# Kernel tuning notes

Hardware: AMD Instinct MI355X
Metric: run time of the kernel (lower is better)

## Reference

```python
import jax, jax.numpy as jnp
import numpy as np

B, C, O, N, T, K = 4, 64, 64, 32768, 4, 9
PAD, DIL = 4, 1  # padding*dilation, dilation
SIGMA = 0.05
EPS_BN = 1e-5


def _gather_ch(x, idx):
    # x: [B, C, N], idx: [B, N] -> gather along last dim per channel
    idx3 = jnp.broadcast_to(idx[:, None, :], x.shape)
    return jnp.take_along_axis(x, idx3, axis=-1)


def _weighted_conv(x, coords, w):
    # x: [B,C,N], coords: [B,3,N], w: [O,C,K]
    xp = jnp.pad(x, ((0, 0), (0, 0), (PAD, PAD)))
    cp = jnp.pad(coords, ((0, 0), (0, 0), (PAD, PAD)))
    win_idx = jnp.arange(N)[:, None] + jnp.arange(K) * DIL  # [N, K]
    win = xp[:, :, win_idx]   # [B,C,N,K]
    cwin = cp[:, :, win_idx]  # [B,3,N,K]
    d = cwin - cwin[:, :, :, K // 2:K // 2 + 1]
    s = jnp.sum(d * d, axis=1)                    # [B,N,K]
    r = jnp.sqrt(jnp.where(s > 0, s, 1.0))
    r = jnp.where(s > 0, r, 0.0)
    wgt = jnp.maximum(1.0 - r / SIGMA, 0.0)       # [B,N,K]
    return jnp.einsum('bcnk,bnk,ock->bon', win, wgt, w)


def _bn(x, g, b):
    # training-mode BatchNorm1d over (B, N)
    m = jnp.mean(x, axis=(0, 2), keepdims=True)
    v = jnp.var(x, axis=(0, 2), keepdims=True)
    return g[None, :, None] * (x - m) * jax.lax.rsqrt(v + EPS_BN) + b[None, :, None]


def setup_inputs() -> dict:
    key = jax.random.key(0)
    ks = jax.random.split(key, 12)
    inp = jax.random.normal(ks[0], (B, C, N), dtype=jnp.float32)
    # coords in a small box so sigma=0.05 yields non-trivial weights
    multi_coords = jax.random.uniform(ks[1], (B, 3, N, T), dtype=jnp.float32) * 0.02
    indices = jax.random.randint(ks[2], (B, N, T), 0, N, dtype=jnp.int32)
    reindices = jax.random.randint(ks[3], (B, N, T), 0, N, dtype=jnp.int32)
    fan = C * K
    conv_w = jax.random.normal(ks[4], (T, O, C, K), dtype=jnp.float32) / np.sqrt(fan)
    bn_gamma = jnp.ones((T, O), dtype=jnp.float32)
    bn_beta = jnp.zeros((T, O), dtype=jnp.float32)
    fusion_w = jax.random.normal(ks[5], (O, T * O), dtype=jnp.float32) / np.sqrt(T * O)
    fusion_b = jnp.zeros((O,), dtype=jnp.float32)
    fusion_gamma = jnp.ones((O,), dtype=jnp.float32)
    fusion_beta = jnp.zeros((O,), dtype=jnp.float32)
    return {"input": inp, "multi_coords": multi_coords, "indices": indices,
            "reindices": reindices, "conv_w": conv_w, "bn_gamma": bn_gamma,
            "bn_beta": bn_beta, "fusion_w": fusion_w, "fusion_b": fusion_b,
            "fusion_gamma": fusion_gamma, "fusion_beta": fusion_beta}


def reference(input, multi_coords, indices, reindices, conv_w, bn_gamma, bn_beta,
              fusion_w, fusion_b, fusion_gamma, fusion_beta):
    outs = []
    for i in range(T):  # fixed small set of 4 Hilbert orders
        x = _gather_ch(input, indices[:, :, i])            # [B,C,N]
        x = _weighted_conv(x, multi_coords[:, :, :, i], conv_w[i])  # [B,O,N]
        x = _bn(x, bn_gamma[i], bn_beta[i])
        x = _gather_ch(x, reindices[:, :, i])
        outs.append(x)
    cat = jnp.concatenate(outs, axis=1)                    # [B, T*O, N]
    y = jnp.einsum('bcn,oc->bon', cat, fusion_w) + fusion_b[None, :, None]
    y = _bn(y, fusion_gamma, fusion_beta)
    return jax.nn.relu(y)
```

## Files before the change

### kernel.cpp

```cpp
#include <hip/hip_runtime.h>
#include <hip/hip_bf16.h>

#define BB 4
#define CC 64
#define OO 64
#define NN 32768
#define TT 4
#define KK 9
#define PADW 4
#define SIGMA 0.05f
#define EPS_BN 1e-5f

typedef __attribute__((ext_vector_type(8))) short bf16x8;
typedef __attribute__((ext_vector_type(4))) float f32x4;

__device__ __forceinline__ unsigned short f2bf(float f) {
  __hip_bfloat16 h = __float2bfloat16(f);
  return *reinterpret_cast<unsigned short*>(&h);
}
__device__ __forceinline__ unsigned int pkbf(float a, float b) {
  float2 t; t.x = a; t.y = b;
  __hip_bfloat162 h = __float22bfloat162_rn(t);
  unsigned int r;
  __builtin_memcpy(&r, &h, 4);
  return r;
}

__global__ __launch_bounds__(256) void transpose_kernel(
    const float* __restrict__ inp, unsigned short* __restrict__ xTb)
{
  const int n0 = blockIdx.x * 64;
  const int b  = blockIdx.y;
  const int tid = threadIdx.x;
  __shared__ float xt[64][65];
  {
    int nl = tid & 63, c4 = tid >> 6;
    #pragma unroll
    for (int i = 0; i < 16; ++i) {
      int c = c4 * 16 + i;
      xt[c][nl] = inp[((size_t)(b*CC + c))*NN + n0 + nl];
    }
  }
  __syncthreads();
  {
    int nl = tid >> 2, cq = tid & 3;
    unsigned int pk[8];
    #pragma unroll
    for (int i = 0; i < 8; ++i) {
      int c = cq*16 + i*2;
      pk[i] = pkbf(xt[c][nl], xt[c+1][nl]);
    }
    unsigned int* dst = (unsigned int*)(xTb + (((size_t)b*NN) + n0 + nl)*CC + cq*16);
    ((int4*)dst)[0] = make_int4((int)pk[0],(int)pk[1],(int)pk[2],(int)pk[3]);
    ((int4*)dst)[1] = make_int4((int)pk[4],(int)pk[5],(int)pk[6],(int)pk[7]);
  }
}

__global__ __launch_bounds__(256) void wprep_kernel(
    const float* __restrict__ cw, unsigned short* __restrict__ W4)
{
  const int k = blockIdx.x;
  const int t = blockIdx.y;
  for (int u = threadIdx.x; u < OO*CC; u += 256) {
    int o = u >> 6, c = u & 63;
    int ow = o >> 5, ot = (o >> 4) & 1, l15 = o & 15;
    int frag = c >> 5, q = (c >> 3) & 3, j = c & 7;
    float wv = cw[(((size_t)(t*OO + o))*CC + c)*KK + k];
    W4[(size_t)(t*9+k)*4096 + ow*2048 + ot*1024 + frag*512 + l15*32 + q*8 + j]
        = f2bf(wv);
  }
}

__global__ __launch_bounds__(256) void indmc_kernel(
    const int* __restrict__ ind, const float* __restrict__ mc,
    int* __restrict__ indT, float* __restrict__ mcT)
{
  const int n = blockIdx.x * 256 + threadIdx.x;
  const int b = blockIdx.y;
  int4 iv = *(const int4*)(ind + ((size_t)b*NN + n)*TT);
  indT[((size_t)(0*BB + b))*NN + n] = iv.x;
  indT[((size_t)(1*BB + b))*NN + n] = iv.y;
  indT[((size_t)(2*BB + b))*NN + n] = iv.z;
  indT[((size_t)(3*BB + b))*NN + n] = iv.w;
  #pragma unroll
  for (int d = 0; d < 3; ++d) {
    float4 mv = *(const float4*)(mc + (((size_t)(b*3 + d))*NN + n)*TT);
    mcT[((size_t)((0*BB + b)*3 + d))*NN + n] = mv.x;
    mcT[((size_t)((1*BB + b)*3 + d))*NN + n] = mv.y;
    mcT[((size_t)((2*BB + b)*3 + d))*NN + n] = mv.z;
    mcT[((size_t)((3*BB + b)*3 + d))*NN + n] = mv.w;
  }
}

__global__ __launch_bounds__(256, 3) void conv_kernel(
    const unsigned short* __restrict__ xTb,
    const float* __restrict__ mcT,
    const int*   __restrict__ indT,
    const unsigned short* __restrict__ W4,
    unsigned short* __restrict__ Y,
    float* __restrict__ cpart2)
{
  const int n0  = blockIdx.x * 256;
  const int b   = blockIdx.y;
  const int t   = blockIdx.z;
  const int tid = threadIdx.x;
  const int lane = tid & 63;
  const int w    = tid >> 6;
  const int l15  = lane & 15;
  const int q    = lane >> 4;
  const int ow   = w & 1;
  const int nw   = w >> 1;

  __shared__ short xg[264*64];
  __shared__ float wgl[256][10];
  __shared__ float mcs[3][268];
  __shared__ int   ids[268];

  for (int u = tid; u < 264; u += 256) {
    int m = n0 + u - PADW;
    bool v = (m >= 0) && (m < NN);
    ids[u] = v ? indT[((size_t)(t*BB + b))*NN + m] : -1;
    #pragma unroll
    for (int d = 0; d < 3; ++d)
      mcs[d][u] = v ? mcT[((size_t)((t*BB + b)*3 + d))*NN + m] : 0.f;
  }
  __syncthreads();

  int4 g[9];
  #pragma unroll
  for (int i = 0; i < 9; ++i) {
    int u = tid + 256*i;
    g[i] = make_int4(0,0,0,0);
    if (u < 2112) {
      int p = u >> 3, s = u & 7;
      int idx = ids[p];
      if (idx >= 0)
        g[i] = *(const int4*)(xTb + ((size_t)b*NN + idx)*CC + s*8);
    }
  }

  {
    int nl = tid;
    float cx = mcs[0][nl+4], cy = mcs[1][nl+4], cz = mcs[2][nl+4];
    #pragma unroll
    for (int k = 0; k < KK; ++k) {
      float dx = mcs[0][nl+k]-cx, dy = mcs[1][nl+k]-cy, dz = mcs[2][nl+k]-cz;
      float s2 = dx*dx + dy*dy + dz*dz;
      float r = (s2 > 0.f) ? sqrtf(s2) : 0.f;
      wgl[nl][k] = fmaxf(1.f - r*(1.f/SIGMA), 0.f);
    }
  }

  #pragma unroll
  for (int i = 0; i < 9; ++i) {
    int u = tid + 256*i;
    if (u < 2112) {
      int p = u >> 3, s = u & 7;
      *(int4*)&xg[(p << 6) + ((s ^ (p & 7)) << 3)] = g[i];
    }
  }
  __syncthreads();

  const unsigned short* Wt = W4 + (size_t)t*9*4096 + ow*2048 + (l15*4 + q)*8;
  const f32x4 Z = {0.f, 0.f, 0.f, 0.f};
  f32x4 fin[2][8];
  #pragma unroll
  for (int ot = 0; ot < 2; ++ot)
    #pragma unroll
    for (int ns = 0; ns < 8; ++ns) fin[ot][ns] = Z;

  for (int k = 0; k < KK; ++k) {
    const unsigned short* Wk = Wt + (size_t)k*4096;
    bf16x8 af[2][2];
    #pragma unroll
    for (int ot = 0; ot < 2; ++ot) {
      af[ot][0] = *(const bf16x8*)(Wk + ot*1024);
      af[ot][1] = *(const bf16x8*)(Wk + ot*1024 + 512);
    }
    #pragma unroll
    for (int ns = 0; ns < 8; ++ns) {
      int nl = nw*128 + ns*16 + l15;
      int p  = nl + k;
      const short* row = &xg[p << 6];
      int sw = p & 7;
      bf16x8 b0 = *(const bf16x8*)(row + ((q ^ sw) << 3));
      bf16x8 b1 = *(const bf16x8*)(row + (((4 + q) ^ sw) << 3));
      float wgt = wgl[nl][k];
      #pragma unroll
      for (int ot = 0; ot < 2; ++ot) {
        f32x4 d = __builtin_amdgcn_mfma_f32_16x16x32_bf16(af[ot][0], b0, Z, 0, 0, 0);
        d = __builtin_amdgcn_mfma_f32_16x16x32_bf16(af[ot][1], b1, d, 0, 0, 0);
        fin[ot][ns] += wgt * d;
      }
    }
  }

  #pragma unroll
  for (int ns = 0; ns < 8; ++ns) {
    int nl = nw*128 + ns*16 + l15;
    size_t row = (((size_t)t*BB + b)*NN + n0 + nl)*OO;
    #pragma unroll
    for (int ot = 0; ot < 2; ++ot) {
      uint2 pk2;
      pk2.x = pkbf(fin[ot][ns][0], fin[ot][ns][1]);
      pk2.y = pkbf(fin[ot][ns][2], fin[ot][ns][3]);
      *(uint2*)(Y + row + ow*32 + ot*16 + q*4) = pk2;
    }
  }

  float sv[16];
  #pragma unroll
  for (int ot = 0; ot < 2; ++ot)
    #pragma unroll
    for (int r = 0; r < 4; ++r) {
      float a = 0.f, qs = 0.f;
      #pragma unroll
      for (int ns = 0; ns < 8; ++ns) {
        float v = fin[ot][ns][r];
        a += v; qs += v*v;
      }
      sv[ot*4+r] = a; sv[8+ot*4+r] = qs;
    }
  #pragma unroll
  for (int msk = 1; msk < 16; msk <<= 1) {
    #pragma unroll
    for (int i = 0; i < 16; ++i) sv[i] += __shfl_xor(sv[i], msk, 16);
  }
  if (l15 == 0) {
    int slot4 = ((b*128 + (int)blockIdx.x) << 2) | w;
    #pragma unroll
    for (int ot = 0; ot < 2; ++ot)
      #pragma unroll
      for (int r = 0; r < 4; ++r) {
        int o = ow*32 + ot*16 + q*4 + r;
        cpart2[((size_t)((t*64 + o)*2 + 0))*2048 + slot4] = sv[ot*4+r];
        cpart2[((size_t)((t*64 + o)*2 + 1))*2048 + slot4] = sv[8+ot*4+r];
      }
  }
}

__global__ __launch_bounds__(256) void bnparam_kernel(
    const float* __restrict__ cpart2,
    const float* __restrict__ gam,
    const float* __restrict__ bet,
    float* __restrict__ ss)
{
  const int to = blockIdx.x;
  const int tid = threadIdx.x;
  __shared__ float r1[256], r2[256];
  const float* p1 = cpart2 + (size_t)to*2*2048;
  const float* p2 = p1 + 2048;
  float s1 = 0.f, s2 = 0.f;
  for (int i = tid*4; i < 2048; i += 1024) {
    float4 a = *(const float4*)(p1 + i);
    float4 c = *(const float4*)(p2 + i);
    s1 += a.x + a.y + a.z + a.w;
    s2 += c.x + c.y + c.z + c.w;
  }
  r1[tid] = s1; r2[tid] = s2;
  __syncthreads();
  for (int st = 128; st > 0; st >>= 1) {
    if (tid < st) { r1[tid] += r1[tid+st]; r2[tid] += r2[tid+st]; }
    __syncthreads();
  }
  if (tid == 0) {
    const float inv = 1.f / (float)(BB * NN);
    float mean = r1[0] * inv;
    float var  = r2[0] * inv - mean * mean;
    float sc = gam[to] * rsqrtf(var + EPS_BN);
    ss[to*2 + 0] = sc;
    ss[to*2 + 1] = bet[to] - mean * sc;
  }
}

__global__ __launch_bounds__(256) void wfuse_kernel(
    const float* __restrict__ fw,
    const float* __restrict__ fb,
    const float* __restrict__ ss,
    float* __restrict__ fbp,
    unsigned short* __restrict__ FWB)
{
  const int tid = threadIdx.x;
  {
    int o = tid >> 2, c0 = (tid & 3) * 64;
    float s = 0.f;
    for (int c = c0; c < c0 + 64; ++c)
      s += fw[o*256 + c] * ss[c*2 + 1];
    s += __shfl_xor(s, 1);
    s += __shfl_xor(s, 2);
    if ((tid & 3) == 0) fbp[o] = fb[o] + s;
  }
  for (int e = tid; e < 16384; e += 256) {
    int rk  = e >> 11;
    int ow  = (e >> 10) & 1;
    int ot  = (e >> 9) & 1;
    int l15 = (e >> 5) & 15;
    int cj  = e & 31;
    int o = ow*32 + ot*16 + l15;
    int c = (rk >> 1)*64 + (rk & 1)*32 + cj;
    FWB[e] = f2bf(fw[o*256 + c] * ss[c*2]);
  }
}

__global__ __launch_bounds__(256, 6) void fusion_kernel(
    const unsigned short* __restrict__ Y,
    const int*   __restrict__ rind,
    const unsigned short* __restrict__ FWB,
    const float* __restrict__ fbp,
    float* __restrict__ out,
    float* __restrict__ fpart2)
{
  const int n0  = blockIdx.x * 128;
  const int b   = blockIdx.y;
  const int tid = threadIdx.x;
  const int lane = tid & 63;
  const int w    = tid >> 6;
  const int l15  = lane & 15;
  const int q    = lane >> 4;
  const int ow   = w & 1;
  const int nw   = w >> 1;

  __shared__ short zg[128*64];

  int4 rg[4];
  #pragma unroll
  for (int i = 0; i < 4; ++i) {
    int n = (tid >> 3) + 32*i;
    rg[i] = *(const int4*)(rind + ((size_t)b*NN + n0 + n)*TT);
  }

  f32x4 fin[2][4];
  #pragma unroll
  for (int ot = 0; ot < 2; ++ot)
    #pragma unroll
    for (int ns = 0; ns < 4; ++ns) fin[ot][ns] = (f32x4){0.f,0.f,0.f,0.f};

  #pragma unroll
  for (int r = 0; r < 4; ++r) {
    if (r) __syncthreads();
    #pragma unroll
    for (int i = 0; i < 4; ++i) {
      int u = tid + 256*i;
      int n = u >> 3, s = u & 7;
      int rn = (r == 0) ? rg[i].x : (r == 1) ? rg[i].y
             : (r == 2) ? rg[i].z : rg[i].w;
      int4 raw = *(const int4*)(Y + (((size_t)r*BB + b)*NN + rn)*OO + s*8);
      *(int4*)&zg[(n << 6) + ((s ^ (n & 7)) << 3)] = raw;
    }
    __syncthreads();

    #pragma unroll
    for (int kk = 0; kk < 2; ++kk) {
      int rk = r*2 + kk;
      const unsigned short* wp = FWB + rk*2048 + ow*1024 + (l15*4 + q)*8;
      bf16x8 af[2];
      af[0] = *(const bf16x8*)(wp);
      af[1] = *(const bf16x8*)(wp + 512);
      #pragma unroll
      for (int ns = 0; ns < 4; ++ns) {
        int nl = nw*64 + ns*16 + l15;
        int ch = (kk*4 + q) ^ (nl & 7);
        bf16x8 bfr = *(const bf16x8*)&zg[(nl << 6) + (ch << 3)];
        #pragma unroll
        for (int ot = 0; ot < 2; ++ot)
          fin[ot][ns] = __builtin_amdgcn_mfma_f32_16x16x32_bf16(af[ot], bfr, fin[ot][ns], 0, 0, 0);
      }
    }
  }

  float sv[16];
  #pragma unroll
  for (int ot = 0; ot < 2; ++ot)
    #pragma unroll
    for (int r2 = 0; r2 < 4; ++r2) {
      int o = ow*32 + ot*16 + q*4 + r2;
      float bias = fbp[o];
      float* dst = out + ((size_t)(b*OO + o))*NN + n0 + nw*64;
      float a = 0.f, qs = 0.f;
      #pragma unroll
      for (int ns = 0; ns < 4; ++ns) {
        float v = fin[ot][ns][r2] + bias;
        dst[ns*16 + l15] = v;
        a += v; qs += v*v;
      }
      sv[ot*4+r2] = a; sv[8+ot*4+r2] = qs;
    }
  #pragma unroll
  for (int msk = 1; msk < 16; msk <<= 1) {
    #pragma unroll
    for (int i = 0; i < 16; ++i) sv[i] += __shfl_xor(sv[i], msk, 16);
  }
  if (l15 == 0) {
    int slot4 = ((b*256 + (int)blockIdx.x) << 2) | w;
    #pragma unroll
    for (int ot = 0; ot < 2; ++ot)
      #pragma unroll
      for (int r2 = 0; r2 < 4; ++r2) {
        int o = ow*32 + ot*16 + q*4 + r2;
        fpart2[((size_t)(o*2 + 0))*4096 + slot4] = sv[ot*4+r2];
        fpart2[((size_t)(o*2 + 1))*4096 + slot4] = sv[8+ot*4+r2];
      }
  }
}

__global__ __launch_bounds__(256) void freduce_kernel(
    const float* __restrict__ fpart2,
    const float* __restrict__ fg,
    const float* __restrict__ fbeta,
    float* __restrict__ fss)
{
  const int o = blockIdx.x;
  const int tid = threadIdx.x;
  __shared__ float r1[256], r2[256];
  const float* p1 = fpart2 + (size_t)o*2*4096;
  const float* p2 = p1 + 4096;
  float s1 = 0.f, s2 = 0.f;
  for (int i = tid*4; i < 4096; i += 1024) {
    float4 a = *(const float4*)(p1 + i);
    float4 c = *(const float4*)(p2 + i);
    s1 += a.x + a.y + a.z + a.w;
    s2 += c.x + c.y + c.z + c.w;
  }
  r1[tid] = s1; r2[tid] = s2;
  __syncthreads();
  for (int st = 128; st > 0; st >>= 1) {
    if (tid < st) { r1[tid] += r1[tid+st]; r2[tid] += r2[tid+st]; }
    __syncthreads();
  }
  if (tid == 0) {
    const float inv = 1.f / (float)(BB * NN);
    float mean = r1[0] * inv;
    float var  = r2[0] * inv - mean * mean;
    float sc = fg[o] * rsqrtf(var + EPS_BN);
    fss[o*2 + 0] = sc;
    fss[o*2 + 1] = fbeta[o] - mean * sc;
  }
}

__global__ __launch_bounds__(256) void final_kernel(
    float* __restrict__ out, const float* __restrict__ fss)
{
  const int e0 = blockIdx.x * 2048 + threadIdx.x;
  #pragma unroll
  for (int s = 0; s < 8; ++s) {
    int e  = e0 + s * 256;
    int o2 = (e >> 15) & 63;
    float sc = fss[o2*2 + 0];
    float sh = fss[o2*2 + 1];
    float v = out[e] * sc + sh;
    out[e] = fmaxf(v, 0.f);
  }
}

extern "C" void kernel_launch(void* const* d_in, const int* in_sizes, int n_in,
                              void* d_out, int out_size, void* d_ws, size_t ws_size,
                              hipStream_t stream) {
  const float* inp  = (const float*)d_in[0];
  const float* mc   = (const float*)d_in[1];
  const int*   ind  = (const int*)  d_in[2];
  const int*   rind = (const int*)  d_in[3];
  const float* cw   = (const float*)d_in[4];
  const float* bg   = (const float*)d_in[5];
  const float* bb   = (const float*)d_in[6];
  const float* fw   = (const float*)d_in[7];
  const float* fb   = (const float*)d_in[8];
  const float* fg   = (const float*)d_in[9];
  const float* fbt  = (const float*)d_in[10];

  char* ws = (char*)d_ws;
  float* convss = (float*)(ws + 0);
  float* fss    = (float*)(ws + 2048);
  float* fbp    = (float*)(ws + 3072);
  unsigned short* Y = (unsigned short*)(ws + 8192);
  float* fpart2 = (float*)(ws + 8192 + 67108864);
  unsigned short* FWB = (unsigned short*)(ws + 8192 + 67108864 + 2097152);

  char* ob = (char*)d_out;
  unsigned short* xTb = (unsigned short*)ob;
  unsigned short* W4  = (unsigned short*)(ob + 16777216);
  float* cpart2 = (float*)(ob + 17072128);
  int*   indT   = (int*)  (ob + 21266432);
  float* mcT    = (float*)(ob + 23363584);
  float* out = (float*)d_out;

  dim3 gt(NN/64, BB);
  transpose_kernel<<<gt, 256, 0, stream>>>(inp, xTb);

  dim3 gw(KK, TT);
  wprep_kernel<<<gw, 256, 0, stream>>>(cw, W4);

  dim3 gi(NN/256, BB);
  indmc_kernel<<<gi, 256, 0, stream>>>(ind, mc, indT, mcT);

  dim3 gc(NN/256, BB, TT);
  conv_kernel<<<gc, 256, 0, stream>>>(xTb, mcT, indT, W4, Y, cpart2);

  bnparam_kernel<<<256, 256, 0, stream>>>(cpart2, bg, bb, convss);

  wfuse_kernel<<<1, 256, 0, stream>>>(fw, fb, convss, fbp, FWB);

  dim3 gf(NN/128, BB);
  fusion_kernel<<<gf, 256, 0, stream>>>(Y, rind, FWB, fbp, out, fpart2);

  freduce_kernel<<<OO, 256, 0, stream>>>(fpart2, fg, fbt, fss);

  final_kernel<<<(BB*OO*NN)/2048, 256, 0, stream>>>(out, fss);
}
```

Baseline: 224.6 us.

## Merge prep kernels into one launch, gather indices via registers, lower fusion occupancy

Combines the transpose, weight-prep and index/coord transpose kernels into a single launch whose block ID selects the branch, cutting two kernel launches and their gaps. In the conv kernel, each thread now loads its gather indices from global memory straight into registers and issues the feature gathers before the shared-memory barrier, so the dependent loads are no longer serialized behind an LDS round trip and sync. The fusion kernel's minimum-blocks hint drops from 6 to 4, which allows more registers per thread at the cost of occupancy. Each thread now reads indices redundantly (8 lanes per point), which adds some global traffic.

```diff
diff --git a/kernel.cpp b/kernel.cpp
--- a/kernel.cpp
+++ b/kernel.cpp
@@ -26,69 +26,69 @@
   return r;
 }
 
-__global__ __launch_bounds__(256) void transpose_kernel(
-    const float* __restrict__ inp, unsigned short* __restrict__ xTb)
-{
-  const int n0 = blockIdx.x * 64;
-  const int b  = blockIdx.y;
+__global__ __launch_bounds__(256) void prep_kernel(
+    const float* __restrict__ inp, unsigned short* __restrict__ xTb,
+    const float* __restrict__ cw,  unsigned short* __restrict__ W4,
+    const int*   __restrict__ ind, const float* __restrict__ mc,
+    int* __restrict__ indT, float* __restrict__ mcT)
+{
+  __shared__ float xt[64][65];
+  const int bid = blockIdx.x;
   const int tid = threadIdx.x;
-  __shared__ float xt[64][65];
-  {
-    int nl = tid & 63, c4 = tid >> 6;
-    #pragma unroll
-    for (int i = 0; i < 16; ++i) {
-      int c = c4 * 16 + i;
-      xt[c][nl] = inp[((size_t)(b*CC + c))*NN + n0 + nl];
-    }
-  }
-  __syncthreads();
-  {
-    int nl = tid >> 2, cq = tid & 3;
-    unsigned int pk[8];
-    #pragma unroll
-    for (int i = 0; i < 8; ++i) {
-      int c = cq*16 + i*2;
-      pk[i] = pkbf(xt[c][nl], xt[c+1][nl]);
-    }
-    unsigned int* dst = (unsigned int*)(xTb + (((size_t)b*NN) + n0 + nl)*CC + cq*16);
-    ((int4*)dst)[0] = make_int4((int)pk[0],(int)pk[1],(int)pk[2],(int)pk[3]);
-    ((int4*)dst)[1] = make_int4((int)pk[4],(int)pk[5],(int)pk[6],(int)pk[7]);
-  }
-}
-
-__global__ __launch_bounds__(256) void wprep_kernel(
-    const float* __restrict__ cw, unsigned short* __restrict__ W4)
-{
-  const int k = blockIdx.x;
-  const int t = blockIdx.y;
-  for (int u = threadIdx.x; u < OO*CC; u += 256) {
-    int o = u >> 6, c = u & 63;
-    int ow = o >> 5, ot = (o >> 4) & 1, l15 = o & 15;
-    int frag = c >> 5, q = (c >> 3) & 3, j = c & 7;
-    float wv = cw[(((size_t)(t*OO + o))*CC + c)*KK + k];
-    W4[(size_t)(t*9+k)*4096 + ow*2048 + ot*1024 + frag*512 + l15*32 + q*8 + j]
-        = f2bf(wv);
-  }
-}
-
-__global__ __launch_bounds__(256) void indmc_kernel(
-    const int* __restrict__ ind, const float* __restrict__ mc,
-    int* __restrict__ indT, float* __restrict__ mcT)
-{
-  const int n = blockIdx.x * 256 + threadIdx.x;
-  const int b = blockIdx.y;
-  int4 iv = *(const int4*)(ind + ((size_t)b*NN + n)*TT);
-  indT[((size_t)(0*BB + b))*NN + n] = iv.x;
-  indT[((size_t)(1*BB + b))*NN + n] = iv.y;
-  indT[((size_t)(2*BB + b))*NN + n] = iv.z;
-  indT[((size_t)(3*BB + b))*NN + n] = iv.w;
-  #pragma unroll
-  for (int d = 0; d < 3; ++d) {
-    float4 mv = *(const float4*)(mc + (((size_t)(b*3 + d))*NN + n)*TT);
-    mcT[((size_t)((0*BB + b)*3 + d))*NN + n] = mv.x;
-    mcT[((size_t)((1*BB + b)*3 + d))*NN + n] = mv.y;
-    mcT[((size_t)((2*BB + b)*3 + d))*NN + n] = mv.z;
-    mcT[((size_t)((3*BB + b)*3 + d))*NN + n] = mv.w;
+
+  if (bid < 2048) {
+    const int n0 = (bid & 511) * 64;
+    const int b  = bid >> 9;
+    {
+      int nl = tid & 63, c4 = tid >> 6;
+      #pragma unroll
+      for (int i = 0; i < 16; ++i) {
+        int c = c4 * 16 + i;
+        xt[c][nl] = inp[((size_t)(b*CC + c))*NN + n0 + nl];
+      }
+    }
+    __syncthreads();
+    {
+      int nl = tid >> 2, cq = tid & 3;
+      unsigned int pk[8];
+      #pragma unroll
+      for (int i = 0; i < 8; ++i) {
+        int c = cq*16 + i*2;
+        pk[i] = pkbf(xt[c][nl], xt[c+1][nl]);
+      }
+      unsigned int* dst = (unsigned int*)(xTb + (((size_t)b*NN) + n0 + nl)*CC + cq*16);
+      ((int4*)dst)[0] = make_int4((int)pk[0],(int)pk[1],(int)pk[2],(int)pk[3]);
+      ((int4*)dst)[1] = make_int4((int)pk[4],(int)pk[5],(int)pk[6],(int)pk[7]);
+    }
+  } else if (bid < 2560) {
+    const int id = bid - 2048;
+    const int n  = (id & 127) * 256 + tid;
+    const int b  = id >> 7;
+    int4 iv = *(const int4*)(ind + ((size_t)b*NN + n)*TT);
+    indT[((size_t)(0*BB + b))*NN + n] = iv.x;
+    indT[((size_t)(1*BB + b))*NN + n] = iv.y;
+    indT[((size_t)(2*BB + b))*NN + n] = iv.z;
+    indT[((size_t)(3*BB + b))*NN + n] = iv.w;
+    #pragma unroll
+    for (int d = 0; d < 3; ++d) {
+      float4 mv = *(const float4*)(mc + (((size_t)(b*3 + d))*NN + n)*TT);
+      mcT[((size_t)((0*BB + b)*3 + d))*NN + n] = mv.x;
+      mcT[((size_t)((1*BB + b)*3 + d))*NN + n] = mv.y;
+      mcT[((size_t)((2*BB + b)*3 + d))*NN + n] = mv.z;
+      mcT[((size_t)((3*BB + b)*3 + d))*NN + n] = mv.w;
+    }
+  } else {
+    const int id = bid - 2560;
+    const int k = id % KK;
+    const int t = id / KK;
+    for (int u = tid; u < OO*CC; u += 256) {
+      int o = u >> 6, c = u & 63;
+      int ow = o >> 5, ot = (o >> 4) & 1, l15 = o & 15;
+      int frag = c >> 5, q = (c >> 3) & 3, j = c & 7;
+      float wv = cw[(((size_t)(t*OO + o))*CC + c)*KK + k];
+      W4[(size_t)(t*9+k)*4096 + ow*2048 + ot*1024 + frag*512 + l15*32 + q*8 + j]
+          = f2bf(wv);
+    }
   }
 }
 
@@ -114,30 +114,35 @@
   __shared__ short xg[264*64];
   __shared__ float wgl[256][10];
   __shared__ float mcs[3][268];
-  __shared__ int   ids[268];
+
+  int idxr[9];
+  #pragma unroll
+  for (int i = 0; i < 9; ++i) {
+    int u = tid + 256*i;
+    int p = u >> 3;
+    int m = n0 + p - PADW;
+    idxr[i] = -1;
+    if (u < 2112 && m >= 0 && m < NN)
+      idxr[i] = indT[((size_t)(t*BB + b))*NN + m];
+  }
+
+  int4 g[9];
+  #pragma unroll
+  for (int i = 0; i < 9; ++i) {
+    int s = (tid + 256*i) & 7;
+    g[i] = make_int4(0,0,0,0);
+    if (idxr[i] >= 0)
+      g[i] = *(const int4*)(xTb + ((size_t)b*NN + idxr[i])*CC + s*8);
+  }
 
   for (int u = tid; u < 264; u += 256) {
     int m = n0 + u - PADW;
     bool v = (m >= 0) && (m < NN);
-    ids[u] = v ? indT[((size_t)(t*BB + b))*NN + m] : -1;
     #pragma unroll
     for (int d = 0; d < 3; ++d)
       mcs[d][u] = v ? mcT[((size_t)((t*BB + b)*3 + d))*NN + m] : 0.f;
   }
   __syncthreads();
-
-  int4 g[9];
-  #pragma unroll
-  for (int i = 0; i < 9; ++i) {
-    int u = tid + 256*i;
-    g[i] = make_int4(0,0,0,0);
-    if (u < 2112) {
-      int p = u >> 3, s = u & 7;
-      int idx = ids[p];
-      if (idx >= 0)
-        g[i] = *(const int4*)(xTb + ((size_t)b*NN + idx)*CC + s*8);
-    }
-  }
 
   {
     int nl = tid;
@@ -302,7 +307,7 @@
   }
 }
 
-__global__ __launch_bounds__(256, 6) void fusion_kernel(
+__global__ __launch_bounds__(256, 4) void fusion_kernel(
     const unsigned short* __restrict__ Y,
     const int*   __restrict__ rind,
     const unsigned short* __restrict__ FWB,
@@ -483,14 +488,7 @@
   float* mcT    = (float*)(ob + 23363584);
   float* out = (float*)d_out;
 
-  dim3 gt(NN/64, BB);
-  transpose_kernel<<<gt, 256, 0, stream>>>(inp, xTb);
-
-  dim3 gw(KK, TT);
-  wprep_kernel<<<gw, 256, 0, stream>>>(cw, W4);
-
-  dim3 gi(NN/256, BB);
-  indmc_kernel<<<gi, 256, 0, stream>>>(ind, mc, indT, mcT);
+  prep_kernel<<<2596, 256, 0, stream>>>(inp, xTb, cw, W4, ind, mc, indT, mcT);
 
   dim3 gc(NN/256, BB, TT);
   conv_kernel<<<gc, 256, 0, stream>>>(xTb, mcT, indT, W4, Y, cpart2);
```

Result: faster. 218.1 us (-2.9%).
